# Kernel optimization log

Measured on AMD Instinct MI355X. Metric: run time of the kernel, lower is better.

The kernel has to match this reference:

```python
import jax, jax.numpy as jnp
import numpy as np

K = 11
EPS = 1e-6


def _box_sum(a):
    # a: [B, H, W] -> KxK zero-padded local sum (equivalent to nn.Unfold padding=K//2 then sum)
    return jax.lax.reduce_window(a, 0.0, jax.lax.add,
                                 window_dimensions=(1, K, K),
                                 window_strides=(1, 1, 1),
                                 padding='SAME')


def setup_inputs() -> dict:
    key = jax.random.key(0)
    k1, k2 = jax.random.split(key)
    x = jax.random.normal(k1, (8, 3, 1024, 1024), dtype=jnp.float32)
    y = jax.random.normal(k2, (8, 3, 1024, 1024), dtype=jnp.float32)
    return {"x": x, "y": y}


def reference(x, y):
    # Channel-reduce first, then local KxK box sums (math-identical to the
    # unfold-based sum over (C, K, K) with zero padding).
    xx = _box_sum((x * x).sum(axis=1))   # [B, H, W]
    yy = _box_sum((y * y).sum(axis=1))
    xy = _box_sum((x * y).sum(axis=1))
    x_norm = jnp.sqrt(xx)
    y_norm = jnp.sqrt(yy)
    return xy / (x_norm * y_norm + EPS)
```

## Files before the change

kernel.cpp:

```cpp
#include <hip/hip_runtime.h>
#include <math.h>

#define NB 8
#define NC 3
#define NH 1024
#define NW 1024
#define EPS 1e-6f

#define BAND 128
#define CH 16
#define KSTEPS (CH + 10)
#define PADW 144

__global__ __launch_bounds__(64, 2)
void lcs_kernel(const float* __restrict__ x, const float* __restrict__ y,
                float* __restrict__ out) {
    __shared__ __align__(16) float P[3][PADW];

    const int l   = threadIdx.x;
    const int bid = blockIdx.x;
    const int b     = bid >> 9;
    const int rem   = bid & 511;
    const int band0 = (rem & 7) * BAND;
    const int r0    = (rem >> 3) * CH;

    const size_t chan = (size_t)NH * NW;
    const float* xb = x + (size_t)b * NC * chan;
    const float* yb = y + (size_t)b * NC * chan;

    const int gc0 = band0 - 8 + 2 * l;
    const int gcE = band0 + 120 + 2 * l;
    const float mm = (gc0 >= 0) ? 1.f : 0.f;
    const float me = (l < 8 && gcE + 1 <= NW - 1) ? 1.f : 0.f;
    const int o0 = (gc0 >= 0) ? gc0 : 0;
    const int oE = (me > 0.f) ? gcE : 0;

    float2 cur[12], nxt[12];
    auto ldrow = [&](int gr, float2* d) {
        const int rc = gr < 0 ? 0 : (gr > NH - 1 ? NH - 1 : gr);
        const size_t ro = (size_t)rc * NW;
        #pragma unroll
        for (int c = 0; c < 3; ++c) {
            const float* xr = xb + c * chan + ro;
            const float* yr = yb + c * chan + ro;
            d[c]     = *(const float2*)(xr + o0);
            d[3 + c] = *(const float2*)(yr + o0);
            d[6 + c] = *(const float2*)(xr + oE);
            d[9 + c] = *(const float2*)(yr + oE);
        }
    };

    ldrow(r0 - 5, cur);

    float2 ring[3][11];
    #pragma unroll
    for (int p = 0; p < 3; ++p)
        #pragma unroll
        for (int s = 0; s < 11; ++s) ring[p][s] = make_float2(0.f, 0.f);
    float2 vs[3] = {make_float2(0.f,0.f), make_float2(0.f,0.f), make_float2(0.f,0.f)};

    for (int g = 0; g < 3; ++g) {
        #pragma unroll
        for (int s = 0; s < 11; ++s) {
            const int k = g * 11 + s;
            if (k >= KSTEPS) continue;

            if (k + 1 < KSTEPS) ldrow(r0 - 4 + k, nxt);

            float2 pxx = make_float2(0.f,0.f), pyy = pxx, pxy = pxx;
            float2 qxx = pxx, qyy = pxx, qxy = pxx;
            #pragma unroll
            for (int c = 0; c < 3; ++c) {
                const float2 xm = cur[c],   ym = cur[3+c];
                const float2 xe = cur[6+c], ye = cur[9+c];
                pxx.x += xm.x*xm.x; pxx.y += xm.y*xm.y;
                pyy.x += ym.x*ym.x; pyy.y += ym.y*ym.y;
                pxy.x += xm.x*ym.x; pxy.y += xm.y*ym.y;
                qxx.x += xe.x*xe.x; qxx.y += xe.y*xe.y;
                qyy.x += ye.x*ye.x; qyy.y += ye.y*ye.y;
                qxy.x += xe.x*ye.x; qxy.y += xe.y*ye.y;
            }
            const int gr = r0 - 5 + k;
            const float rmf = (gr >= 0 && gr < NH) ? 1.f : 0.f;
            const float cmM = rmf * mm, cmE = rmf * me;
            pxx.x *= cmM; pxx.y *= cmM; pyy.x *= cmM; pyy.y *= cmM;
            pxy.x *= cmM; pxy.y *= cmM;
            qxx.x *= cmE; qxx.y *= cmE; qyy.x *= cmE; qyy.y *= cmE;
            qxy.x *= cmE; qxy.y *= cmE;

            ((float2*)&P[0][0])[l] = pxx;
            ((float2*)&P[1][0])[l] = pyy;
            ((float2*)&P[2][0])[l] = pxy;
            if (l < 8) {
                ((float2*)&P[0][0])[64 + l] = qxx;
                ((float2*)&P[1][0])[64 + l] = qyy;
                ((float2*)&P[2][0])[64 + l] = qxy;
            }
            __builtin_amdgcn_wave_barrier();

            #pragma unroll
            for (int p = 0; p < 3; ++p) {
                const float* Pp = &P[p][0];
                float2 t[7];
                #pragma unroll
                for (int j = 0; j < 7; ++j)
                    t[j] = *(const float2*)(Pp + 2*l + 2 + 2*j);
                float h0 = ((t[0].y + t[1].x) + (t[1].y + t[2].x))
                         + ((t[2].y + t[3].x) + (t[3].y + t[4].x))
                         + ((t[4].y + t[5].x) + t[5].y);
                float h1 = h0 - t[0].y + t[6].x;
                vs[p].x += h0 - ring[p][s].x;
                vs[p].y += h1 - ring[p][s].y;
                ring[p][s].x = h0;
                ring[p][s].y = h1;
            }
            __builtin_amdgcn_wave_barrier();

            if (k >= 10) {
                const int orow = r0 + k - 10;
                const float d0 = __builtin_amdgcn_sqrtf(vs[0].x) *
                                 __builtin_amdgcn_sqrtf(vs[1].x) + EPS;
                const float d1 = __builtin_amdgcn_sqrtf(vs[0].y) *
                                 __builtin_amdgcn_sqrtf(vs[1].y) + EPS;
                float2 o;
                o.x = vs[2].x * __builtin_amdgcn_rcpf(d0);
                o.y = vs[2].y * __builtin_amdgcn_rcpf(d1);
                *(float2*)(out + ((size_t)b * NH + orow) * NW + band0 + 2*l) = o;
            }

            if (k + 1 < KSTEPS) {
                #pragma unroll
                for (int i = 0; i < 12; ++i) cur[i] = nxt[i];
            }
        }
    }
}

extern "C" void kernel_launch(void* const* d_in, const int* in_sizes, int n_in,
                              void* d_out, int out_size, void* d_ws, size_t ws_size,
                              hipStream_t stream) {
    const float* x = (const float*)d_in[0];
    const float* y = (const float*)d_in[1];
    float* out = (float*)d_out;
    lcs_kernel<<<dim3(4096), dim3(64), 0, stream>>>(x, y, out);
}
```

Measured before the change: 256.9 us.

## Split fused kernel into horizontal-pass and vertical-pass kernels via workspace

Adds a two-kernel path. The first kernel reduces channels and computes the 11-wide horizontal box sums per row into a three-plane workspace. The second kernel does the 11-tall vertical running sum with a register ring and writes the normalized output. This removes the redundant row-halo reloads and the small 64-thread blocks of the fused kernel, at the cost of an extra workspace write and read. It falls back to the old kernel when the workspace is too small.

```diff
diff --git a/kernel.cpp b/kernel.cpp
--- a/kernel.cpp
+++ b/kernel.cpp
@@ -6,6 +6,121 @@
 #define NH 1024
 #define NW 1024
 #define EPS 1e-6f
+
+#define WS_PLANE ((size_t)NB * NH * NW)
+
+__global__ __launch_bounds__(256, 4)
+void lcs_hpass(const float* __restrict__ x, const float* __restrict__ y,
+               float* __restrict__ ws) {
+    __shared__ __align__(16) float Pp[3][1040];
+
+    const int t   = threadIdx.x;
+    const int bid = blockIdx.x;
+    const int b   = bid >> 8;
+    const int rg  = bid & 255;
+
+    #pragma unroll
+    for (int p = 0; p < 3; ++p) {
+        if (t < 8)  Pp[p][t] = 0.f;
+        if (t < 8)  Pp[p][1032 + t] = 0.f;
+    }
+
+    const size_t chan = (size_t)NH * NW;
+    const float* xb = x + (size_t)b * NC * chan;
+    const float* yb = y + (size_t)b * NC * chan;
+    float* wsb = ws + (size_t)b * chan;
+
+    for (int rr = 0; rr < 4; ++rr) {
+        const int row = rg * 4 + rr;
+        const size_t ro = (size_t)row * NW + 4 * t;
+
+        float4 pxx = make_float4(0.f,0.f,0.f,0.f), pyy = pxx, pxy = pxx;
+        #pragma unroll
+        for (int c = 0; c < 3; ++c) {
+            const float4 fx = *(const float4*)(xb + c * chan + ro);
+            const float4 fy = *(const float4*)(yb + c * chan + ro);
+            pxx.x += fx.x*fx.x; pxx.y += fx.y*fx.y; pxx.z += fx.z*fx.z; pxx.w += fx.w*fx.w;
+            pyy.x += fy.x*fy.x; pyy.y += fy.y*fy.y; pyy.z += fy.z*fy.z; pyy.w += fy.w*fy.w;
+            pxy.x += fx.x*fy.x; pxy.y += fx.y*fy.y; pxy.z += fx.z*fy.z; pxy.w += fx.w*fy.w;
+        }
+
+        __syncthreads();
+        *(float4*)&Pp[0][8 + 4*t] = pxx;
+        *(float4*)&Pp[1][8 + 4*t] = pyy;
+        *(float4*)&Pp[2][8 + 4*t] = pxy;
+        __syncthreads();
+
+        const float4 own[3] = {pxx, pyy, pxy};
+        #pragma unroll
+        for (int p = 0; p < 3; ++p) {
+            const float* q = &Pp[p][0];
+            const float  wm1 = q[4*t + 3];
+            const float4 A   = *(const float4*)(q + 4*t + 4);
+            const float4 B   = own[p];
+            const float4 C   = *(const float4*)(q + 4*t + 12);
+            const float  wp  = q[4*t + 16];
+            float4 h;
+            h.x = wm1 + ((A.x + A.y) + (A.z + A.w))
+                      + ((B.x + B.y) + (B.z + B.w)) + (C.x + C.y);
+            h.y = h.x - wm1 + C.z;
+            h.z = h.y - A.x + C.w;
+            h.w = h.z - A.y + wp;
+            *(float4*)(wsb + (size_t)p * WS_PLANE + ro) = h;
+        }
+    }
+}
+
+#define CHB 32
+#define KSB (CHB + 10)
+
+__global__ __launch_bounds__(256, 4)
+void lcs_vpass(const float* __restrict__ ws, float* __restrict__ out) {
+    const int t   = threadIdx.x;
+    const int bid = blockIdx.x;
+    const int b   = bid >> 7;
+    const int rem = bid & 127;
+    const int cg  = rem & 3;
+    const int rc  = rem >> 2;
+    const int col = cg * 256 + t;
+    const int r0  = rc * CHB;
+
+    const float* base = ws + (size_t)b * NH * NW + col;
+
+    float ring[3][11];
+    #pragma unroll
+    for (int p = 0; p < 3; ++p)
+        #pragma unroll
+        for (int s = 0; s < 11; ++s) ring[p][s] = 0.f;
+    float sxx = 0.f, syy = 0.f, sxy = 0.f;
+
+    for (int g = 0; g < 4; ++g) {
+        #pragma unroll
+        for (int s = 0; s < 11; ++s) {
+            const int k = g * 11 + s;
+            if (k >= KSB) continue;
+            const int h = r0 - 5 + k;
+
+            float vxx = 0.f, vyy = 0.f, vxy = 0.f;
+            if (h >= 0 && h < NH) {
+                const size_t off = (size_t)h * NW;
+                vxx = base[0 * WS_PLANE + off];
+                vyy = base[1 * WS_PLANE + off];
+                vxy = base[2 * WS_PLANE + off];
+            }
+            sxx += vxx - ring[0][s]; ring[0][s] = vxx;
+            syy += vyy - ring[1][s]; ring[1][s] = vyy;
+            sxy += vxy - ring[2][s]; ring[2][s] = vxy;
+
+            if (k >= 10) {
+                const int r = r0 + k - 10;
+                const float den = __builtin_amdgcn_sqrtf(sxx) *
+                                  __builtin_amdgcn_sqrtf(syy) + EPS;
+                out[((size_t)b * NH + r) * NW + col] =
+                    sxy * __builtin_amdgcn_rcpf(den);
+            }
+        }
+    }
+}
 
 #define BAND 128
 #define CH 16
@@ -64,7 +179,6 @@
         for (int s = 0; s < 11; ++s) {
             const int k = g * 11 + s;
             if (k >= KSTEPS) continue;
-
             if (k + 1 < KSTEPS) ldrow(r0 - 4 + k, nxt);
 
             float2 pxx = make_float2(0.f,0.f), pyy = pxx, pxy = pxx;
@@ -101,14 +215,14 @@
             #pragma unroll
             for (int p = 0; p < 3; ++p) {
                 const float* Pp = &P[p][0];
-                float2 t[7];
+                float2 tt[7];
                 #pragma unroll
                 for (int j = 0; j < 7; ++j)
-                    t[j] = *(const float2*)(Pp + 2*l + 2 + 2*j);
-                float h0 = ((t[0].y + t[1].x) + (t[1].y + t[2].x))
-                         + ((t[2].y + t[3].x) + (t[3].y + t[4].x))
-                         + ((t[4].y + t[5].x) + t[5].y);
-                float h1 = h0 - t[0].y + t[6].x;
+                    tt[j] = *(const float2*)(Pp + 2*l + 2 + 2*j);
+                float h0 = ((tt[0].y + tt[1].x) + (tt[1].y + tt[2].x))
+                         + ((tt[2].y + tt[3].x) + (tt[3].y + tt[4].x))
+                         + ((tt[4].y + tt[5].x) + tt[5].y);
+                float h1 = h0 - tt[0].y + tt[6].x;
                 vs[p].x += h0 - ring[p][s].x;
                 vs[p].y += h1 - ring[p][s].y;
                 ring[p][s].x = h0;
@@ -127,7 +241,6 @@
                 o.y = vs[2].y * __builtin_amdgcn_rcpf(d1);
                 *(float2*)(out + ((size_t)b * NH + orow) * NW + band0 + 2*l) = o;
             }
-
             if (k + 1 < KSTEPS) {
                 #pragma unroll
                 for (int i = 0; i < 12; ++i) cur[i] = nxt[i];
@@ -142,5 +255,13 @@
     const float* x = (const float*)d_in[0];
     const float* y = (const float*)d_in[1];
     float* out = (float*)d_out;
-    lcs_kernel<<<dim3(4096), dim3(64), 0, stream>>>(x, y, out);
-}
+
+    const size_t need = (size_t)3 * NB * NH * NW * sizeof(float);
+    if (d_ws != nullptr && ws_size >= need) {
+        float* ws = (float*)d_ws;
+        lcs_hpass<<<dim3(NB * 256), dim3(256), 0, stream>>>(x, y, ws);
+        lcs_vpass<<<dim3(1024),     dim3(256), 0, stream>>>(ws, out);
+    } else {
+        lcs_kernel<<<dim3(4096), dim3(64), 0, stream>>>(x, y, out);
+    }
+}
```

Result: no change. 260.8 us (+1.5%).
